# Performance work log

Measured on AMD Instinct MI355X. Metric: run time of the kernel, lower is better.

Reference implementation:

```python
import jax, jax.numpy as jnp
import numpy as np

B, T = 64, 1000
Q_DIM, M_DIM, A_DIM = 1024, 512, 128
N_FILT, KSIZE = 32, 31
PAD = (KSIZE - 1) // 2


def setup_inputs() -> dict:
    key = jax.random.key(0)
    ks = jax.random.split(key, 12)
    inp = {
        "query": jax.random.normal(ks[0], (B, Q_DIM), dtype=jnp.float32),
        "memory": jax.random.normal(ks[1], (B, T, M_DIM), dtype=jnp.float32),
        "attention_weights_cum": jax.random.uniform(ks[2], (B, 1, T), dtype=jnp.float32),
        "mask": jnp.zeros((B, T), dtype=bool),
        # params (Linear weights stored [out, in] like torch)
        "Wq": jax.random.normal(ks[3], (A_DIM, Q_DIM), dtype=jnp.float32) * 0.03,
        "bq": jnp.zeros((A_DIM,), dtype=jnp.float32),
        "Wm": jax.random.normal(ks[4], (A_DIM, M_DIM), dtype=jnp.float32) * 0.04,
        "bm": jnp.zeros((A_DIM,), dtype=jnp.float32),
        "Wv": jax.random.normal(ks[5], (1, A_DIM), dtype=jnp.float32) * 0.09,
        "bv": jnp.zeros((1,), dtype=jnp.float32),
        "conv_w": jax.random.normal(ks[6], (N_FILT, 1, KSIZE), dtype=jnp.float32) * 0.18,
        "conv_b": jnp.zeros((N_FILT,), dtype=jnp.float32),
        "Wloc": jax.random.normal(ks[7], (A_DIM, N_FILT), dtype=jnp.float32) * 0.18,
    }
    return inp


def reference(query, memory, attention_weights_cum, mask,
              Wq, bq, Wm, bm, Wv, bv, conv_w, conv_b, Wloc):
    # key projection: [B, T, A]
    key = jnp.einsum('btm,am->bta', memory, Wm) + bm
    # query projection: [B, 1, A]
    q = (query @ Wq.T + bq)[:, None, :]
    # location conv: [B,1,T] -> [B,N_FILT,T]
    loc = jax.lax.conv_general_dilated(
        attention_weights_cum, conv_w, window_strides=(1,),
        padding=[(PAD, PAD)], dimension_numbers=('NCH', 'OIH', 'NCH'))
    loc = loc + conv_b[None, :, None]
    # [B, T, A]
    loc = jnp.einsum('bft,af->bta', loc, Wloc)
    # energies: [B, T]
    energies = (jnp.tanh(q + loc + key) @ Wv.T + bv)[..., 0]
    alignment = jnp.where(mask, -jnp.inf, energies)
    attention_weights = jax.nn.softmax(alignment, axis=1)  # [B, T]
    attention_context = jnp.einsum('bt,btm->bm', attention_weights, memory)
    return attention_context, attention_weights
```

## Files before the change

kernel.cpp:

```cpp
#include <hip/hip_runtime.h>
#include <math.h>

#define Bsz 64
#define Tn 1000
#define QD 1024
#define MD 512
#define AD 128
#define NF 32
#define KS 31
#define PADc 15

#define NCH 16
#define RPC 64
#define SUB 16
#define ROWSH 520

typedef __attribute__((ext_vector_type(8))) short bf16x8;
typedef __attribute__((ext_vector_type(4))) float f32x4;

#define OFF_ENERG 32768
#define OFF_WMF  288768
#define OFF_W2F  419840
#define OFF_ML   428032
#define OFF_CTXC 436224
#define OFF_MEMB 2533376

static __device__ __forceinline__ short f2bf(float x) {
    unsigned u = __float_as_uint(x);
    unsigned r = (u + 0x7fffu + ((u >> 16) & 1u)) >> 16;
    return (short)r;
}
static __device__ __forceinline__ float bf2f(short s) {
    return __uint_as_float(((unsigned)(unsigned short)s) << 16);
}
static __device__ __forceinline__ float fast_tanh(float x) {
    float e2 = __expf(2.f * x);
    return 1.f - 2.f / (e2 + 1.f);
}

__global__ __launch_bounds__(256)
void k_convert(const float* __restrict__ mem, short* __restrict__ memB) {
    int g = blockIdx.x * 256 + threadIdx.x;
#pragma unroll
    for (int u = 0; u < 8; ++u) {
        size_t e = (size_t)(g + u * 524288) * 8;
        if (e < (size_t)Bsz * Tn * MD) {
            float4 v0 = *(const float4*)(mem + e);
            float4 v1 = *(const float4*)(mem + e + 4);
            bf16x8 o;
            o[0] = f2bf(v0.x); o[1] = f2bf(v0.y); o[2] = f2bf(v0.z); o[3] = f2bf(v0.w);
            o[4] = f2bf(v1.x); o[5] = f2bf(v1.y); o[6] = f2bf(v1.z); o[7] = f2bf(v1.w);
            *(bf16x8*)(memB + e) = o;
        }
    }
}

__global__ __launch_bounds__(256)
void k_prep(const float* __restrict__ Wm, const float* __restrict__ conv_w,
            const float* __restrict__ conv_b, const float* __restrict__ Wloc,
            const float* __restrict__ query, const float* __restrict__ Wq,
            const float* __restrict__ bq, const float* __restrict__ bm,
            short* __restrict__ WmF, short* __restrict__ W2F,
            float* __restrict__ qsum) {
    __shared__ float qs[QD];
    __shared__ float red[256];
    int bid = blockIdx.x;
    if (bid < 32) {
        int g = bid * 256 + threadIdx.x;
        int wc = g >> 6, l = g & 63;
        int a = (wc >> 4) * 16 + (l & 15);
        int kb = (wc & 15) * 32 + (l >> 4) * 8;
        const float* src = Wm + a * MD + kb;
        float4 v0 = *(const float4*)src;
        float4 v1 = *(const float4*)(src + 4);
        bf16x8 o;
        o[0] = f2bf(v0.x); o[1] = f2bf(v0.y); o[2] = f2bf(v0.z); o[3] = f2bf(v0.w);
        o[4] = f2bf(v1.x); o[5] = f2bf(v1.y); o[6] = f2bf(v1.z); o[7] = f2bf(v1.w);
        *(bf16x8*)(WmF + (size_t)g * 8) = o;
    } else if (bid < 96) {
        int b = bid - 32;
        int a = threadIdx.x & 127;
        int half = threadIdx.x >> 7;
        for (int i = threadIdx.x; i < QD; i += 256) qs[i] = query[b * QD + i];
        __syncthreads();
        const float4* Wq4 = (const float4*)(Wq + a * QD + half * (QD / 2));
        const float4* qs4 = (const float4*)(qs + half * (QD / 2));
        float acc = 0.f;
#pragma unroll 4
        for (int i = 0; i < QD / 8; ++i) {
            float4 w = Wq4[i];
            float4 q = qs4[i];
            acc += w.x * q.x + w.y * q.y + w.z * q.z + w.w * q.w;
        }
        red[threadIdx.x] = acc;
        __syncthreads();
        if (half == 0) {
            float b2 = 0.f;
            for (int f = 0; f < NF; ++f) b2 += conv_b[f] * Wloc[a * NF + f];
            qsum[b * AD + a] = red[a] + red[a + 128] + bq[a] + bm[a] + b2;
        }
    } else {
        for (int s = threadIdx.x * 2; s < threadIdx.x * 2 + 2; ++s) {
            int w = s >> 6, l = s & 63;
            int a = w * 16 + (l & 15);
            int kb = (l >> 4) * 8;
            bf16x8 o;
#pragma unroll
            for (int j = 0; j < 8; ++j) {
                int k = kb + j;
                float sum = 0.f;
                if (k < KS)
                    for (int f = 0; f < NF; ++f) sum += conv_w[f * KS + k] * Wloc[a * NF + f];
                o[j] = f2bf(sum);
            }
            *(bf16x8*)(W2F + s * 8) = o;
        }
    }
}

__global__ __launch_bounds__(512)
void k_fused(const short* __restrict__ memB, const float* __restrict__ awc,
             const unsigned char* __restrict__ mask,
             const short* __restrict__ WmF, const short* __restrict__ W2F,
             const float* __restrict__ Wv, const float* __restrict__ bv,
             const float* __restrict__ qsum, float* __restrict__ energ,
             float* __restrict__ ctxc, float2* __restrict__ ml) {
    __shared__ __align__(16) short chunk[RPC * ROWSH];
    __shared__ float ered[8][SUB + 1];
    __shared__ float Esub[RPC];
    __shared__ float ps[RPC];
    __shared__ float vmask[RPC];
    __shared__ short awcsB[96];

    const int b = blockIdx.y, c = blockIdx.x;
    const int t0 = c * RPC;
    const int tid = threadIdx.x;
    const int w = tid >> 6, lane = tid & 63, m16 = lane & 15, q = lane >> 4;

    bf16x8 bf[17];
#pragma unroll
    for (int cc = 0; cc < 16; ++cc) bf[cc] = ((const bf16x8*)WmF)[(w * 16 + cc) * 64 + lane];
    bf[16] = ((const bf16x8*)W2F)[w * 64 + lane];

    const int a = w * 16 + m16;
    const float wvv = Wv[a];
    const float qsv = qsum[b * AD + a];
    const float bv0 = bv[0];

    if (tid < 96) {
        int g = t0 - PADc + tid;
        float v = (tid <= 94 && g >= 0 && g < Tn) ? awc[b * Tn + g] : 0.f;
        awcsB[tid] = f2bf(v);
    }
    if (tid < RPC) {
        int t = t0 + tid;
        bool valid = (t < Tn) && (mask[b * Tn + (t < Tn ? t : 0)] == 0);
        vmask[tid] = valid ? 1.f : 0.f;
    }

#pragma unroll
    for (int s = 0; s < 4; ++s) {
#pragma unroll
        for (int rr = 0; rr < 2; ++rr) {
            int row = s * SUB + w * 2 + rr;
            int t = t0 + row;
            int tc = t < Tn ? t : Tn - 1;
            const short* gp = memB + (((size_t)b * Tn + tc) << 9) + lane * 8;
            short* lp = &chunk[row * ROWSH] + lane * 8;
            __builtin_amdgcn_global_load_lds(
                (const __attribute__((address_space(1))) void*)gp,
                (__attribute__((address_space(3))) void*)lp, 16, 0, 0);
        }
    }

    asm volatile("s_waitcnt lgkmcnt(0)" ::: "memory");
    __builtin_amdgcn_s_barrier();

#pragma unroll
    for (int s = 0; s < 4; ++s) {
        switch (s) {
            case 0: asm volatile("s_waitcnt vmcnt(6)" ::: "memory"); break;
            case 1: asm volatile("s_waitcnt vmcnt(4)" ::: "memory"); break;
            case 2: asm volatile("s_waitcnt vmcnt(2)" ::: "memory"); break;
            default: asm volatile("s_waitcnt vmcnt(0)" ::: "memory"); break;
        }
        __builtin_amdgcn_s_barrier();

        f32x4 acc = (f32x4){0.f, 0.f, 0.f, 0.f};
        const short* arow = &chunk[(s * SUB + m16) * ROWSH + q * 8];
#pragma unroll
        for (int cc = 0; cc < 16; ++cc) {
            bf16x8 af = *(const bf16x8*)(arow + cc * 32);
            acc = __builtin_amdgcn_mfma_f32_16x16x32_bf16(af, bf[cc], acc, 0, 0, 0);
        }
        {
            int tl = s * SUB + m16;
            bf16x8 af;
#pragma unroll
            for (int j = 0; j < 8; ++j) af[j] = awcsB[tl + q * 8 + j];
            acc = __builtin_amdgcn_mfma_f32_16x16x32_bf16(af, bf[16], acc, 0, 0, 0);
        }

#pragma unroll
        for (int r = 0; r < 4; ++r) {
            float e = wvv * fast_tanh(acc[r] + qsv);
#pragma unroll
            for (int m2 = 1; m2 < 16; m2 <<= 1) e += __shfl_xor(e, m2, 64);
            if (m16 == 0) ered[w][q * 4 + r] = e;
        }
        asm volatile("s_waitcnt lgkmcnt(0)" ::: "memory");
        __builtin_amdgcn_s_barrier();
        if (tid < SUB) {
            float E = bv0;
#pragma unroll
            for (int ww = 0; ww < 8; ++ww) E += ered[ww][tid];
            Esub[s * SUB + tid] = E;
        }
    }

    asm volatile("s_waitcnt lgkmcnt(0)" ::: "memory");
    __builtin_amdgcn_s_barrier();

    float mx = -1e30f;
#pragma unroll
    for (int r = 0; r < RPC; ++r) {
        float e = (vmask[r] != 0.f) ? Esub[r] : -1e30f;
        mx = fmaxf(mx, e);
    }
    if (tid < RPC) ps[tid] = vmask[tid] * __expf(Esub[tid] - mx);
    asm volatile("s_waitcnt lgkmcnt(0)" ::: "memory");
    __builtin_amdgcn_s_barrier();

    float ctxj = 0.f, psum = 0.f;
#pragma unroll 8
    for (int r = 0; r < RPC; ++r) {
        float p = ps[r];
        psum += p;
        ctxj += p * bf2f(chunk[r * ROWSH + tid]);
    }
    ctxc[((size_t)c * Bsz + b) * MD + tid] = ctxj;
    if (tid < RPC) {
        int t = t0 + tid;
        if (t < Tn) energ[b * Tn + t] = Esub[tid];
    }
    if (tid == 0) ml[c * Bsz + b] = make_float2(mx, psum);
}

__global__ __launch_bounds__(512)
void k_combine(const float* __restrict__ ctxc, const float2* __restrict__ ml,
               const float* __restrict__ energ, const unsigned char* __restrict__ mask,
               float* __restrict__ ctx, float* __restrict__ wout) {
    __shared__ float sm[NCH], sl[NCH];
    int b = blockIdx.x;
    int tid = threadIdx.x;
    if (tid < NCH) {
        float2 v = ml[tid * Bsz + b];
        sm[tid] = v.x;
        sl[tid] = v.y;
    }
    __syncthreads();
    float M = -1e30f;
#pragma unroll
    for (int cc = 0; cc < NCH; ++cc) M = fmaxf(M, sm[cc]);
    float L = 0.f;
#pragma unroll
    for (int cc = 0; cc < NCH; ++cc) L += sl[cc] * __expf(sm[cc] - M);
    float inv = 1.f / L;

    float s = 0.f;
#pragma unroll
    for (int cc = 0; cc < NCH; ++cc)
        s += ctxc[((size_t)cc * Bsz + b) * MD + tid] * __expf(sm[cc] - M);
    ctx[b * MD + tid] = s * inv;

#pragma unroll
    for (int i = 0; i < 2; ++i) {
        int t = tid + i * 512;
        if (t < Tn) {
            bool msk = mask[b * Tn + t] != 0;
            float e = energ[b * Tn + t];
            wout[b * Tn + t] = msk ? 0.f : __expf(e - M) * inv;
        }
    }
}

extern "C" void kernel_launch(void* const* d_in, const int* in_sizes, int n_in,
                              void* d_out, int out_size, void* d_ws, size_t ws_size,
                              hipStream_t stream) {
    const float* query  = (const float*)d_in[0];
    const float* memory = (const float*)d_in[1];
    const float* awc    = (const float*)d_in[2];
    const unsigned char* mask = (const unsigned char*)d_in[3];
    const float* Wq     = (const float*)d_in[4];
    const float* bq     = (const float*)d_in[5];
    const float* Wm     = (const float*)d_in[6];
    const float* bm     = (const float*)d_in[7];
    const float* Wv     = (const float*)d_in[8];
    const float* bv     = (const float*)d_in[9];
    const float* conv_w = (const float*)d_in[10];
    const float* conv_b = (const float*)d_in[11];
    const float* Wloc   = (const float*)d_in[12];

    float* out = (float*)d_out;
    float* ctx = out;
    float* wout = out + Bsz * MD;

    float* qsum  = (float*)d_ws;
    float* energ = (float*)((char*)d_ws + OFF_ENERG);
    short* WmF   = (short*)((char*)d_ws + OFF_WMF);
    short* W2F   = (short*)((char*)d_ws + OFF_W2F);
    float2* ml   = (float2*)((char*)d_ws + OFF_ML);
    float* ctxc  = (float*)((char*)d_ws + OFF_CTXC);
    short* memB  = (short*)((char*)d_ws + OFF_MEMB);

    k_prep<<<dim3(97), dim3(256), 0, stream>>>(Wm, conv_w, conv_b, Wloc, query, Wq,
                                               bq, bm, WmF, W2F, qsum);
    k_convert<<<dim3(2048), dim3(256), 0, stream>>>(memory, memB);
    k_fused<<<dim3(NCH, Bsz), dim3(512), 0, stream>>>(
        memB, awc, mask, WmF, W2F, Wv, bv, qsum, energ, ctxc, ml);
    k_combine<<<dim3(Bsz), dim3(512), 0, stream>>>(ctxc, ml, energ, mask, ctx, wout);
}
```

Baseline: 275.9 us.

## Fuse fp32-to-bf16 memory conversion into main attention kernel

Removes the separate conversion kernel that wrote a bf16 copy of memory to workspace. The fused kernel now loads fp32 memory rows directly into registers, double-buffered across sub-chunks, then converts and stores them to LDS before the MFMA stage. This drops a full read and write pass over the 131 MB memory tensor and one kernel launch. In exchange it adds register pressure, sets an occupancy hint of 4 blocks on launch bounds, and replaces asynchronous global-to-LDS loads with register staging.

```diff
diff --git a/kernel.cpp b/kernel.cpp
--- a/kernel.cpp
+++ b/kernel.cpp
@@ -23,7 +23,6 @@
 #define OFF_W2F  419840
 #define OFF_ML   428032
 #define OFF_CTXC 436224
-#define OFF_MEMB 2533376
 
 static __device__ __forceinline__ short f2bf(float x) {
     unsigned u = __float_as_uint(x);
@@ -36,23 +35,6 @@
 static __device__ __forceinline__ float fast_tanh(float x) {
     float e2 = __expf(2.f * x);
     return 1.f - 2.f / (e2 + 1.f);
-}
-
-__global__ __launch_bounds__(256)
-void k_convert(const float* __restrict__ mem, short* __restrict__ memB) {
-    int g = blockIdx.x * 256 + threadIdx.x;
-#pragma unroll
-    for (int u = 0; u < 8; ++u) {
-        size_t e = (size_t)(g + u * 524288) * 8;
-        if (e < (size_t)Bsz * Tn * MD) {
-            float4 v0 = *(const float4*)(mem + e);
-            float4 v1 = *(const float4*)(mem + e + 4);
-            bf16x8 o;
-            o[0] = f2bf(v0.x); o[1] = f2bf(v0.y); o[2] = f2bf(v0.z); o[3] = f2bf(v0.w);
-            o[4] = f2bf(v1.x); o[5] = f2bf(v1.y); o[6] = f2bf(v1.z); o[7] = f2bf(v1.w);
-            *(bf16x8*)(memB + e) = o;
-        }
-    }
 }
 
 __global__ __launch_bounds__(256)
@@ -118,8 +100,8 @@
     }
 }
 
-__global__ __launch_bounds__(512)
-void k_fused(const short* __restrict__ memB, const float* __restrict__ awc,
+__global__ __launch_bounds__(512, 4)
+void k_fused(const float* __restrict__ mem, const float* __restrict__ awc,
              const unsigned char* __restrict__ mask,
              const short* __restrict__ WmF, const short* __restrict__ W2F,
              const float* __restrict__ Wv, const float* __restrict__ bv,
@@ -158,32 +140,43 @@
         vmask[tid] = valid ? 1.f : 0.f;
     }
 
+    const float* gbase = mem + (size_t)b * Tn * MD + lane * 8;
+    float4 stg[2][2][2];
+#pragma unroll
+    for (int rr = 0; rr < 2; ++rr) {
+        int t = t0 + w * 2 + rr;
+        int tc = t < Tn ? t : Tn - 1;
+        const float* p = gbase + (size_t)tc * MD;
+        stg[0][rr][0] = *(const float4*)p;
+        stg[0][rr][1] = *(const float4*)(p + 4);
+    }
+
+    asm volatile("s_waitcnt lgkmcnt(0)" ::: "memory");
+    __builtin_amdgcn_s_barrier();
+
 #pragma unroll
     for (int s = 0; s < 4; ++s) {
 #pragma unroll
         for (int rr = 0; rr < 2; ++rr) {
             int row = s * SUB + w * 2 + rr;
-            int t = t0 + row;
-            int tc = t < Tn ? t : Tn - 1;
-            const short* gp = memB + (((size_t)b * Tn + tc) << 9) + lane * 8;
-            short* lp = &chunk[row * ROWSH] + lane * 8;
-            __builtin_amdgcn_global_load_lds(
-                (const __attribute__((address_space(1))) void*)gp,
-                (__attribute__((address_space(3))) void*)lp, 16, 0, 0);
-        }
-    }
-
-    asm volatile("s_waitcnt lgkmcnt(0)" ::: "memory");
-    __builtin_amdgcn_s_barrier();
-
-#pragma unroll
-    for (int s = 0; s < 4; ++s) {
-        switch (s) {
-            case 0: asm volatile("s_waitcnt vmcnt(6)" ::: "memory"); break;
-            case 1: asm volatile("s_waitcnt vmcnt(4)" ::: "memory"); break;
-            case 2: asm volatile("s_waitcnt vmcnt(2)" ::: "memory"); break;
-            default: asm volatile("s_waitcnt vmcnt(0)" ::: "memory"); break;
-        }
+            float4 v0 = stg[s & 1][rr][0];
+            float4 v1 = stg[s & 1][rr][1];
+            bf16x8 o;
+            o[0] = f2bf(v0.x); o[1] = f2bf(v0.y); o[2] = f2bf(v0.z); o[3] = f2bf(v0.w);
+            o[4] = f2bf(v1.x); o[5] = f2bf(v1.y); o[6] = f2bf(v1.z); o[7] = f2bf(v1.w);
+            *(bf16x8*)(&chunk[row * ROWSH] + lane * 8) = o;
+        }
+        if (s < 3) {
+#pragma unroll
+            for (int rr = 0; rr < 2; ++rr) {
+                int t = t0 + (s + 1) * SUB + w * 2 + rr;
+                int tc = t < Tn ? t : Tn - 1;
+                const float* p = gbase + (size_t)tc * MD;
+                stg[(s + 1) & 1][rr][0] = *(const float4*)p;
+                stg[(s + 1) & 1][rr][1] = *(const float4*)(p + 4);
+            }
+        }
+        asm volatile("s_waitcnt lgkmcnt(0)" ::: "memory");
         __builtin_amdgcn_s_barrier();
 
         f32x4 acc = (f32x4){0.f, 0.f, 0.f, 0.f};
@@ -311,12 +304,10 @@
     short* W2F   = (short*)((char*)d_ws + OFF_W2F);
     float2* ml   = (float2*)((char*)d_ws + OFF_ML);
     float* ctxc  = (float*)((char*)d_ws + OFF_CTXC);
-    short* memB  = (short*)((char*)d_ws + OFF_MEMB);
 
     k_prep<<<dim3(97), dim3(256), 0, stream>>>(Wm, conv_w, conv_b, Wloc, query, Wq,
                                                bq, bm, WmF, W2F, qsum);
-    k_convert<<<dim3(2048), dim3(256), 0, stream>>>(memory, memB);
     k_fused<<<dim3(NCH, Bsz), dim3(512), 0, stream>>>(
-        memB, awc, mask, WmF, W2F, Wv, bv, qsum, energ, ctxc, ml);
+        memory, awc, mask, WmF, W2F, Wv, bv, qsum, energ, ctxc, ml);
     k_combine<<<dim3(Bsz), dim3(512), 0, stream>>>(ctxc, ml, energ, mask, ctx, wout);
 }
```

Measured after the change: 245.4 us. 1.12x faster.
